# Kernel optimization log

Hardware: AMD Instinct MI355X
Metric: run time of the kernel (lower is better)

Reference implementation:

```python
import jax, jax.numpy as jnp
import numpy as np

D_ATOM, D_MODEL, H = 128, 512, 4
D_H = D_ATOM // H
D_FF = 4 * D_ATOM
EPS = 1e-5


def _ln(x, g, b):
    m = jnp.mean(x, axis=-1, keepdims=True)
    v = jnp.mean((x - m) ** 2, axis=-1, keepdims=True)
    return (x - m) / jnp.sqrt(v + EPS) * g + b


def setup_inputs() -> dict:
    key = jax.random.key(0)
    ks = jax.random.split(key, 20)
    B, N_ATOM, N_PAIRS, N_TOK = 2, 2048, 16384, 512
    c_atom = jax.random.normal(ks[0], (B, N_ATOM, D_ATOM), dtype=jnp.float32)
    p_lm = jax.random.normal(ks[1], (B, N_PAIRS, 16), dtype=jnp.float32)
    p_lm_idx = jax.random.randint(ks[2], (B, N_PAIRS, 2), 0, N_ATOM, dtype=jnp.int32)
    token_idx = jnp.sort(jax.random.randint(ks[3], (B, N_ATOM), 0, N_TOK, dtype=jnp.int32), axis=-1)
    s = 0.05
    w = lambda k, sh: jax.random.normal(k, sh, dtype=jnp.float32) * s
    return {
        'c_atom': c_atom, 'p_lm': p_lm, 'p_lm_idx': p_lm_idx,
        'token_idx': token_idx, 'n_tokens': N_TOK,
        'ln_attn_g': jnp.ones((D_ATOM,), jnp.float32), 'ln_attn_b': jnp.zeros((D_ATOM,), jnp.float32),
        'w_q': w(ks[4], (D_ATOM, D_ATOM)), 'w_k': w(ks[5], (D_ATOM, D_ATOM)),
        'w_v': w(ks[6], (D_ATOM, D_ATOM)), 'w_g': w(ks[7], (D_ATOM, D_ATOM)),
        'w_o': w(ks[8], (D_ATOM, D_ATOM)),
        'pb_w': w(ks[9], (16, H)), 'pb_b': jnp.zeros((H,), jnp.float32),
        'ln_ff_g': jnp.ones((D_ATOM,), jnp.float32), 'ln_ff_b': jnp.zeros((D_ATOM,), jnp.float32),
        'sw_w1': w(ks[10], (D_ATOM, D_FF)), 'sw_w2': w(ks[11], (D_ATOM, D_FF)),
        'sw_w3': w(ks[12], (D_FF, D_ATOM)),
        'tok_w': w(ks[13], (D_ATOM, D_MODEL)), 'tok_b': jnp.zeros((D_MODEL,), jnp.float32),
    }


def reference(c_atom, p_lm, p_lm_idx, token_idx, n_tokens,
              ln_attn_g, ln_attn_b, w_q, w_k, w_v, w_g, w_o, pb_w, pb_b,
              ln_ff_g, ln_ff_b, sw_w1, sw_w2, sw_w3, tok_w, tok_b):
    B, N, _ = c_atom.shape
    q_n = _ln(c_atom, ln_attn_g, ln_attn_b)
    Q = (q_n @ w_q).reshape(B, N, H, D_H)
    K = (q_n @ w_k).reshape(B, N, H, D_H)
    V = (q_n @ w_v).reshape(B, N, H, D_H)
    G = q_n @ w_g  # (B, N, d_atom)

    scores = jnp.einsum('bihd,bjhd->bhij', Q, K) / jnp.sqrt(jnp.float32(D_H))

    bias = p_lm @ pb_w + pb_b  # (B, P, H)
    def scat(src, dst, b_):
        return jnp.zeros((H, N, N), b_.dtype).at[:, src, dst].set(b_.T)
    pair_bias = jax.vmap(scat)(p_lm_idx[..., 0], p_lm_idx[..., 1], bias)
    scores = scores + pair_bias

    token_mask = token_idx[:, :, None] == token_idx[:, None, :]  # (B,N,N)
    scores = jnp.where(token_mask[:, None], scores, -jnp.inf)
    attn = jax.nn.softmax(scores, axis=-1)
    attn = jnp.nan_to_num(attn)

    att_out = jnp.einsum('bhij,bjhd->bihd', attn, V).reshape(B, N, D_ATOM)
    q = c_atom + jax.nn.sigmoid(G) * (att_out @ w_o)
    h = _ln(q, ln_ff_g, ln_ff_b)
    q = q + (jax.nn.silu(h @ sw_w1) * (h @ sw_w2)) @ sw_w3
    atom_feat = q @ tok_w + tok_b  # (B, N, d_model)

    seg = (token_idx + jnp.arange(B, dtype=token_idx.dtype)[:, None] * n_tokens).reshape(-1)
    sums = jax.ops.segment_sum(atom_feat.reshape(B * N, D_MODEL), seg, num_segments=B * n_tokens)
    cnts = jax.ops.segment_sum(jnp.ones((B * N,), atom_feat.dtype), seg, num_segments=B * n_tokens)
    out = sums / jnp.maximum(cnts, 1.0)[:, None]
    return out.reshape(B, n_tokens, D_MODEL)
```

## Files before the change

### kernel.cpp

```cpp
#include <hip/hip_runtime.h>
#include <hip/hip_bf16.h>
#include <math.h>

#define B_     2
#define N_     2048
#define DA     128
#define H_     4
#define DH     32
#define DFF    512
#define DM     512
#define NT     512
#define NP     16384
#define MAXL   32
#define LDSP   136

typedef short bf16x8 __attribute__((ext_vector_type(8)));
typedef float f32x4  __attribute__((ext_vector_type(4)));

__device__ __forceinline__ short bf16r(float x) {
    union { float f; unsigned u; } v; v.f = x;
    unsigned r = v.u + 0x7FFFu + ((v.u >> 16) & 1u);
    return (short)(r >> 16);
}
__device__ __forceinline__ float bf2f(short h) {
    union { unsigned u; float f; } v;
    v.u = ((unsigned)(unsigned short)h) << 16;
    return v.f;
}

__global__ __launch_bounds__(1024) void setup_kernel(
        const float* __restrict__ wq, const float* __restrict__ wk,
        const float* __restrict__ wv, const float* __restrict__ wg,
        const float* __restrict__ wo, const float* __restrict__ w1,
        const float* __restrict__ w2, const float* __restrict__ w3,
        const float* __restrict__ tw, const int* __restrict__ tok,
        const int* __restrict__ pidx,
        const float* __restrict__ c_atom, const float* __restrict__ lng,
        const float* __restrict__ lnb,
        short* __restrict__ pqkvg, short* __restrict__ pwo,
        short* __restrict__ pw12, short* __restrict__ pw3,
        short* __restrict__ ptok, short* __restrict__ hln,
        int* __restrict__ cnt, int* __restrict__ tst,
        int* __restrict__ win) {
    __shared__ int c[1024];
    __shared__ int sb[1024];
    if (blockIdx.x < 42) {
        int gid = blockIdx.x * 1024 + threadIdx.x;
        int lane = gid & 63;
        int grp = gid >> 6;
        int quad = lane >> 4, nn = lane & 15;
        const float* src; short* dst; int stride;
        if (grp < 128) {
            int g = grp; int kt = g & 3, nt = g >> 2;
            int n = nt * 16 + nn;
            const float* w = (n < 128) ? wq : (n < 256) ? wk : (n < 384) ? wv : wg;
            src = w + (kt * 32 + quad * 8) * 128 + (n & 127);
            dst = pqkvg + (g * 64 + lane) * 8;
            stride = 128;
        } else if (grp < 160) {
            int g = grp - 128; int kt = g & 3, nt = g >> 2;
            src = wo + (kt * 32 + quad * 8) * 128 + nt * 16 + nn;
            dst = pwo + (g * 64 + lane) * 8;
            stride = 128;
        } else if (grp < 416) {
            int g = grp - 160; int kt = g & 3, nt = g >> 2;
            int n = nt * 16 + nn;
            src = ((n & 1) ? w2 : w1) + (kt * 32 + quad * 8) * 512 + (n >> 1);
            dst = pw12 + (g * 64 + lane) * 8;
            stride = 512;
        } else if (grp < 544) {
            int g = grp - 416; int kt = g & 15, nt = g >> 4;
            src = w3 + (kt * 32 + quad * 8) * 128 + nt * 16 + nn;
            dst = pw3 + (g * 64 + lane) * 8;
            stride = 128;
        } else {
            int g = grp - 544; int kt = g & 3, nt = g >> 2;
            src = tw + (kt * 32 + quad * 8) * 512 + nt * 16 + nn;
            dst = ptok + (g * 64 + lane) * 8;
            stride = 512;
        }
#pragma unroll
        for (int j = 0; j < 8; j++) dst[j] = bf16r(src[j * stride]);
    } else if (blockIdx.x == 42) {
        int tid = threadIdx.x;
        c[tid] = 0;
        __syncthreads();
#pragma unroll
        for (int i = 0; i < 4; i++) {
            int idx = tid + i * 1024;
            int b = idx >> 11;
            atomicAdd(&c[b * NT + tok[idx]], 1);
        }
        __syncthreads();
        int t = tid & (NT - 1);
        int v = c[tid];
        int* cur = c;
        int* alt = sb;
        for (int d = 1; d < NT; d <<= 1) {
            int y = cur[tid];
            if (t >= d) y += cur[tid - d];
            alt[tid] = y;
            __syncthreads();
            int* tmp = cur; cur = alt; alt = tmp;
        }
        tst[tid] = cur[tid] - v;
        cnt[tid] = v;
    } else if (blockIdx.x < 75) {
        int p = (blockIdx.x - 43) * 1024 + threadIdx.x;
        int b = p >> 14, pp = p & (NP - 1);
        int src = pidx[p * 2], dst = pidx[p * 2 + 1];
        if (tok[b * N_ + src] == tok[b * N_ + dst])
            atomicMax(&win[(b * N_ + src) * MAXL + (dst & 31)], pp + 1);
    } else {
        int t = threadIdx.x;
        int rowg = (blockIdx.x - 75) * 256 + (t >> 2);
        int sub = t & 3;
        const float* xr = c_atom + rowg * DA + sub * 32;
        float4 v[8];
        float s = 0.f, sq = 0.f;
#pragma unroll
        for (int i = 0; i < 8; i++) {
            v[i] = *(const float4*)(xr + i * 4);
            s  += v[i].x + v[i].y + v[i].z + v[i].w;
            sq += v[i].x * v[i].x + v[i].y * v[i].y + v[i].z * v[i].z + v[i].w * v[i].w;
        }
        s += __shfl_xor(s, 1); sq += __shfl_xor(sq, 1);
        s += __shfl_xor(s, 2); sq += __shfl_xor(sq, 2);
        float mean = s * (1.f / 128.f);
        float var = sq * (1.f / 128.f) - mean * mean;
        float inv = rsqrtf(var + 1e-5f);
        const float* gp = lng + sub * 32;
        const float* bp = lnb + sub * 32;
        short* dst = hln + rowg * DA + sub * 32;
#pragma unroll
        for (int i = 0; i < 8; i++) {
            dst[i * 4 + 0] = bf16r((v[i].x - mean) * inv * gp[i * 4 + 0] + bp[i * 4 + 0]);
            dst[i * 4 + 1] = bf16r((v[i].y - mean) * inv * gp[i * 4 + 1] + bp[i * 4 + 1]);
            dst[i * 4 + 2] = bf16r((v[i].z - mean) * inv * gp[i * 4 + 2] + bp[i * 4 + 2]);
            dst[i * 4 + 3] = bf16r((v[i].w - mean) * inv * gp[i * 4 + 3] + bp[i * 4 + 3]);
        }
    }
}

template<int K, int NTT>
__device__ __forceinline__ void gemm_lds(const short* __restrict__ Alds,
                                         const short* __restrict__ Bp,
                                         int nt0, int lane, f32x4* acc) {
    constexpr int KT = K / 32;
    const short* arow = Alds + (lane & 15) * LDSP + (lane >> 4) * 8;
    const short* bbase = Bp + nt0 * KT * 512 + lane * 8;
#pragma unroll
    for (int kt = 0; kt < KT; kt++) {
        bf16x8 a = *(const bf16x8*)(arow + kt * 32);
#pragma unroll
        for (int nt = 0; nt < NTT; nt++) {
            bf16x8 b = *(const bf16x8*)(bbase + (nt * KT + kt) * 512);
            acc[nt] = __builtin_amdgcn_mfma_f32_16x16x32_bf16(a, b, acc[nt], 0, 0, 0);
        }
    }
}

template<int K, int NTT>
__device__ __forceinline__ void gemm_glb(const short* __restrict__ A,
                                         const short* __restrict__ Bp,
                                         int m0, int nt0, int lane, f32x4* acc) {
    constexpr int KT = K / 32;
    const short* arow = A + (m0 + (lane & 15)) * K + (lane >> 4) * 8;
    const short* bbase = Bp + nt0 * KT * 512 + lane * 8;
#pragma unroll
    for (int kt = 0; kt < KT; kt++) {
        bf16x8 a = *(const bf16x8*)(arow + kt * 32);
#pragma unroll
        for (int nt = 0; nt < NTT; nt++) {
            bf16x8 b = *(const bf16x8*)(bbase + (nt * KT + kt) * 512);
            acc[nt] = __builtin_amdgcn_mfma_f32_16x16x32_bf16(a, b, acc[nt], 0, 0, 0);
        }
    }
}

__global__ __launch_bounds__(256) void qkvg_mfma(const short* __restrict__ hln,
                                                 const short* __restrict__ Bp,
                                                 float* __restrict__ out) {
    int lane = threadIdx.x & 63;
    int wave = threadIdx.x >> 6;
    int m0 = blockIdx.x * 64 + wave * 16;
    int nt0 = blockIdx.y * 8;
    f32x4 acc[8];
#pragma unroll
    for (int i = 0; i < 8; i++)
#pragma unroll
        for (int r = 0; r < 4; r++) acc[i][r] = 0.f;
    gemm_glb<128, 8>(hln, Bp, m0, nt0, lane, acc);
    int r0 = m0 + ((lane >> 4) << 2);
    int cc = lane & 15;
#pragma unroll
    for (int nt = 0; nt < 8; nt++) {
        int col = (nt0 + nt) * 16 + cc;
#pragma unroll
        for (int r = 0; r < 4; r++) out[(r0 + r) * 512 + col] = acc[nt][r];
    }
}

__global__ __launch_bounds__(128) void attn_kernel(const float* __restrict__ qkvg,
                                                   const int* __restrict__ tok,
                                                   const int* __restrict__ tst,
                                                   const int* __restrict__ cnt,
                                                   const int* __restrict__ winner,
                                                   const float* __restrict__ plm,
                                                   const float* __restrict__ pbw,
                                                   const float* __restrict__ pbb,
                                                   short* __restrict__ atth) {
    __shared__ float sc[H_][MAXL];
    int blk = blockIdx.x;
    int b = blk >> 11;
    int h = threadIdx.x >> 5, d = threadIdx.x & 31;
    int t = tok[blk];
    int start = tst[b * NT + t];
    int L = cnt[b * NT + t];
    if (L > MAXL) L = MAXL;
    float qv = qkvg[blk * 512 + h * DH + d];
    const float* kbase = qkvg + (size_t)(b * N_ + start) * 512 + 128 + h * DH + d;
    const float* vbase = kbase + 128;
    const int* wbase = winner + blk * MAXL;
    const float scale = 0.17677669529663687f;
    for (int j0 = 0; j0 < L; j0 += 8) {
        int m = L - j0; if (m > 8) m = 8;
        float kv[8]; int pw[8];
#pragma unroll
        for (int u = 0; u < 8; u++) {
            if (u < m) {
                kv[u] = kbase[(j0 + u) * 512];
                pw[u] = wbase[(start + j0 + u) & 31];
            }
        }
#pragma unroll
        for (int u = 0; u < 8; u++) {
            if (u < m) {
                float s = qv * kv[u];
#pragma unroll
                for (int mm = 16; mm; mm >>= 1) s += __shfl_xor(s, mm, 32);
                s *= scale;
                if (pw[u] > 0) {
                    const float* pl = plm + (size_t)(b * NP + pw[u] - 1) * 16;
                    float bsum = pbb[h];
#pragma unroll
                    for (int f = 0; f < 16; f++) bsum += pl[f] * pbw[f * H_ + h];
                    s += bsum;
                }
                if (d == 0) sc[h][j0 + u] = s;
            }
        }
    }
    __syncthreads();
    float mx = -1e30f;
    for (int jj = 0; jj < L; jj++) mx = fmaxf(mx, sc[h][jj]);
    float denom = 0.f, acc = 0.f;
    for (int j0 = 0; j0 < L; j0 += 8) {
        int m = L - j0; if (m > 8) m = 8;
        float vv[8];
#pragma unroll
        for (int u = 0; u < 8; u++)
            if (u < m) vv[u] = vbase[(j0 + u) * 512];
#pragma unroll
        for (int u = 0; u < 8; u++) {
            if (u < m) {
                float pj = expf(sc[h][j0 + u] - mx);
                denom += pj;
                acc += pj * vv[u];
            }
        }
    }
    atth[blk * DA + h * DH + d] = bf16r(acc / denom);
}

__global__ __launch_bounds__(256) void oplnffn1_mfma(const short* __restrict__ atth,
                                                     const short* __restrict__ pwo,
                                                     const float* __restrict__ qkvg,
                                                     const float* __restrict__ c_atom,
                                                     const float* __restrict__ lg,
                                                     const float* __restrict__ lb,
                                                     const short* __restrict__ pw12,
                                                     float* __restrict__ qbuf,
                                                     short* __restrict__ u) {
    __shared__ short alds[64 * LDSP];
    int lane = threadIdx.x & 63;
    int wave = threadIdx.x >> 6;
    int base = blockIdx.x * 64;
    int m0 = base + wave * 16;
    int quad = lane >> 4, cc = lane & 15;

    f32x4 acc[8];
#pragma unroll
    for (int i = 0; i < 8; i++)
#pragma unroll
        for (int r = 0; r < 4; r++) acc[i][r] = 0.f;
    gemm_glb<128, 8>(atth, pwo, m0, 0, lane, acc);

    float rsum[4], rsq[4];
#pragma unroll
    for (int r = 0; r < 4; r++) {
        int row = m0 + quad * 4 + r;
        float s = 0.f, sq = 0.f;
#pragma unroll
        for (int nt = 0; nt < 8; nt++) {
            int col = nt * 16 + cc;
            float g = qkvg[row * 512 + 384 + col];
            float sg = 1.f / (1.f + expf(-g));
            float val = c_atom[row * DA + col] + sg * acc[nt][r];
            acc[nt][r] = val;
            s += val; sq += val * val;
            if (blockIdx.y == 0) qbuf[row * DA + col] = val;
        }
        rsum[r] = s; rsq[r] = sq;
    }
#pragma unroll
    for (int m = 1; m < 16; m <<= 1) {
#pragma unroll
        for (int r = 0; r < 4; r++) {
            rsum[r] += __shfl_xor(rsum[r], m);
            rsq[r]  += __shfl_xor(rsq[r], m);
        }
    }
#pragma unroll
    for (int r = 0; r < 4; r++) {
        float mean = rsum[r] * (1.f / 128.f);
        float var = rsq[r] * (1.f / 128.f) - mean * mean;
        float inv = rsqrtf(var + 1e-5f);
        int lrow = wave * 16 + quad * 4 + r;
#pragma unroll
        for (int nt = 0; nt < 8; nt++) {
            int col = nt * 16 + cc;
            alds[lrow * LDSP + col] = bf16r((acc[nt][r] - mean) * inv * lg[col] + lb[col]);
        }
    }
    __syncthreads();

    int nt0 = blockIdx.y * 16;
    f32x4 acc2[16];
#pragma unroll
    for (int i = 0; i < 16; i++)
#pragma unroll
        for (int r = 0; r < 4; r++) acc2[i][r] = 0.f;
    gemm_lds<128, 16>(alds + wave * 16 * LDSP, pw12, nt0, lane, acc2);
    int r0 = m0 + quad * 4;
#pragma unroll
    for (int nt = 0; nt < 16; nt++) {
        int col8 = (nt0 + nt) * 8 + (cc >> 1);
#pragma unroll
        for (int r = 0; r < 4; r++) {
            float v = acc2[nt][r];
            float p = __shfl_xor(v, 1);
            if (!(lane & 1)) {
                float sil = v / (1.f + expf(-v));
                u[(r0 + r) * DFF + col8] = bf16r(sil * p);
            }
        }
    }
}

__global__ __launch_bounds__(128) void ffn2_mfma(const short* __restrict__ u,
                                                 const short* __restrict__ Bp,
                                                 const float* __restrict__ qbuf,
                                                 short* __restrict__ q2h) {
    int lane = threadIdx.x & 63;
    int m0 = blockIdx.x * 32 + (threadIdx.x >> 6) * 16;
    int nt0 = blockIdx.y * 2;
    f32x4 acc[2];
#pragma unroll
    for (int i = 0; i < 2; i++)
#pragma unroll
        for (int r = 0; r < 4; r++) acc[i][r] = 0.f;
    gemm_glb<512, 2>(u, Bp, m0, nt0, lane, acc);
    int r0 = m0 + ((lane >> 4) << 2);
    int cc = lane & 15;
#pragma unroll
    for (int nt = 0; nt < 2; nt++) {
        int col = (nt0 + nt) * 16 + cc;
#pragma unroll
        for (int r = 0; r < 4; r++) {
            int row = r0 + r;
            q2h[row * DA + col] = bf16r(qbuf[row * DA + col] + acc[nt][r]);
        }
    }
}

__global__ __launch_bounds__(256) void tokmean_mfma(const short* __restrict__ q2h,
                                                    const int* __restrict__ tst,
                                                    const int* __restrict__ cnt,
                                                    const short* __restrict__ Bp,
                                                    const float* __restrict__ tb,
                                                    float* __restrict__ out) {
    __shared__ short alds[64 * LDSP];
    int tid = threadIdx.x;
    int tt = tid >> 2, sub = tid & 3;
    int token = blockIdx.x * 64 + tt;
    int start = tst[token], n = cnt[token];
    int b = token >> 9;
    float accm[32];
#pragma unroll
    for (int i = 0; i < 32; i++) accm[i] = 0.f;
    const short* rp = q2h + (size_t)(b * N_ + start) * DA + sub * 32;
    if (n > 0) {
        bf16x8 v[4];
#pragma unroll
        for (int v8 = 0; v8 < 4; v8++) v[v8] = *(const bf16x8*)(rp + v8 * 8);
        for (int a = 1; a <= n; a++) {
            bf16x8 nx[4];
            if (a < n) {
#pragma unroll
                for (int v8 = 0; v8 < 4; v8++) nx[v8] = *(const bf16x8*)(rp + a * DA + v8 * 8);
            }
#pragma unroll
            for (int v8 = 0; v8 < 4; v8++)
#pragma unroll
                for (int j = 0; j < 8; j++) accm[v8 * 8 + j] += bf2f(v[v8][j]);
            if (a < n) {
#pragma unroll
                for (int v8 = 0; v8 < 4; v8++) v[v8] = nx[v8];
            }
        }
    }
    float inv = (n > 0) ? 1.f / (float)n : 0.f;
    short* dst = alds + tt * LDSP + sub * 32;
#pragma unroll
    for (int i = 0; i < 32; i++) dst[i] = bf16r(accm[i] * inv);
    __syncthreads();

    int lane = tid & 63;
    int wave = tid >> 6;
    int nt0 = blockIdx.y * 4;
    f32x4 acc[4];
#pragma unroll
    for (int i = 0; i < 4; i++)
#pragma unroll
        for (int r = 0; r < 4; r++) acc[i][r] = 0.f;
    gemm_lds<128, 4>(alds + wave * 16 * LDSP, Bp, nt0, lane, acc);
    int r0 = blockIdx.x * 64 + wave * 16 + ((lane >> 4) << 2);
    int cc = lane & 15;
#pragma unroll
    for (int nt = 0; nt < 4; nt++) {
        int col = (nt0 + nt) * 16 + cc;
        float bv = tb[col];
#pragma unroll
        for (int r = 0; r < 4; r++) out[(size_t)(r0 + r) * DM + col] = acc[nt][r] + bv;
    }
}

extern "C" void kernel_launch(void* const* d_in, const int* in_sizes, int n_in,
                              void* d_out, int out_size, void* d_ws, size_t ws_size,
                              hipStream_t stream) {
    const float* c_atom  = (const float*)d_in[0];
    const float* p_lm    = (const float*)d_in[1];
    const int*   p_idx   = (const int*)d_in[2];
    const int*   tok     = (const int*)d_in[3];
    const float* ln_a_g  = (const float*)d_in[5];
    const float* ln_a_b  = (const float*)d_in[6];
    const float* w_q     = (const float*)d_in[7];
    const float* w_k     = (const float*)d_in[8];
    const float* w_v     = (const float*)d_in[9];
    const float* w_g     = (const float*)d_in[10];
    const float* w_o     = (const float*)d_in[11];
    const float* pb_w    = (const float*)d_in[12];
    const float* pb_b    = (const float*)d_in[13];
    const float* ln_f_g  = (const float*)d_in[14];
    const float* ln_f_b  = (const float*)d_in[15];
    const float* sw_w1   = (const float*)d_in[16];
    const float* sw_w2   = (const float*)d_in[17];
    const float* sw_w3   = (const float*)d_in[18];
    const float* tok_w   = (const float*)d_in[19];
    const float* tok_b   = (const float*)d_in[20];
    float* out = (float*)d_out;

    float* ws = (float*)d_ws;
    int*   cnt   = (int*)ws;
    int*   tst   = cnt + 1024;
    int*   win   = tst + 1024;
    short* pqkvg = (short*)(win + 131072);
    short* pwo   = pqkvg + 65536;
    short* pw12  = pwo + 16384;
    short* pw3   = pw12 + 131072;
    short* ptok  = pw3 + 65536;
    short* atth  = ptok + 65536;
    float* qbuf  = (float*)(atth + 524288);
    float* qkvg  = qbuf + 524288;
    short* uh    = (short*)(qkvg + 2097152);
    short* hln   = uh + 2097152;
    short* q2h   = atth;

    setup_kernel<<<91, 1024, 0, stream>>>(w_q, w_k, w_v, w_g, w_o, sw_w1, sw_w2,
                                          sw_w3, tok_w, tok, p_idx,
                                          c_atom, ln_a_g, ln_a_b,
                                          pqkvg, pwo, pw12, pw3, ptok, hln,
                                          cnt, tst, win);

    qkvg_mfma<<<dim3(64, 4), 256, 0, stream>>>(hln, pqkvg, qkvg);

    attn_kernel<<<B_ * N_, 128, 0, stream>>>(qkvg, tok, tst, cnt, win,
                                             p_lm, pb_w, pb_b, atth);

    oplnffn1_mfma<<<dim3(64, 4), 256, 0, stream>>>(atth, pwo, qkvg, c_atom,
                                                   ln_f_g, ln_f_b, pw12, qbuf, uh);

    ffn2_mfma<<<dim3(128, 4), 128, 0, stream>>>(uh, pw3, qbuf, q2h);

    tokmean_mfma<<<dim3(16, 8), 256, 0, stream>>>(q2h, tst, cnt, ptok, tok_b, out);
}
```

Baseline: 167.6 us.

## Fuse all stages into one cooperative persistent kernel with grid syncs

Replaces the six separate kernel launches with a single cooperative kernel of 256 blocks that runs setup, QKVG GEMM, attention, FFN and token-mean stages separated by grid-wide barriers. Each stage's work is remapped onto the fixed grid, and attention switches to an online softmax that reads K and V in one pass. This aims to remove launch overhead and inter-kernel gaps, at the cost of grid.sync barriers and a fixed grid that may underutilize the device in some stages.

```diff
diff --git a/kernel.cpp b/kernel.cpp
--- a/kernel.cpp
+++ b/kernel.cpp
@@ -1,6 +1,9 @@
 #include <hip/hip_runtime.h>
+#include <hip/hip_cooperative_groups.h>
 #include <hip/hip_bf16.h>
 #include <math.h>
+
+namespace cg = cooperative_groups;
 
 #define B_     2
 #define N_     2048
@@ -28,120 +31,6 @@
     return v.f;
 }
 
-__global__ __launch_bounds__(1024) void setup_kernel(
-        const float* __restrict__ wq, const float* __restrict__ wk,
-        const float* __restrict__ wv, const float* __restrict__ wg,
-        const float* __restrict__ wo, const float* __restrict__ w1,
-        const float* __restrict__ w2, const float* __restrict__ w3,
-        const float* __restrict__ tw, const int* __restrict__ tok,
-        const int* __restrict__ pidx,
-        const float* __restrict__ c_atom, const float* __restrict__ lng,
-        const float* __restrict__ lnb,
-        short* __restrict__ pqkvg, short* __restrict__ pwo,
-        short* __restrict__ pw12, short* __restrict__ pw3,
-        short* __restrict__ ptok, short* __restrict__ hln,
-        int* __restrict__ cnt, int* __restrict__ tst,
-        int* __restrict__ win) {
-    __shared__ int c[1024];
-    __shared__ int sb[1024];
-    if (blockIdx.x < 42) {
-        int gid = blockIdx.x * 1024 + threadIdx.x;
-        int lane = gid & 63;
-        int grp = gid >> 6;
-        int quad = lane >> 4, nn = lane & 15;
-        const float* src; short* dst; int stride;
-        if (grp < 128) {
-            int g = grp; int kt = g & 3, nt = g >> 2;
-            int n = nt * 16 + nn;
-            const float* w = (n < 128) ? wq : (n < 256) ? wk : (n < 384) ? wv : wg;
-            src = w + (kt * 32 + quad * 8) * 128 + (n & 127);
-            dst = pqkvg + (g * 64 + lane) * 8;
-            stride = 128;
-        } else if (grp < 160) {
-            int g = grp - 128; int kt = g & 3, nt = g >> 2;
-            src = wo + (kt * 32 + quad * 8) * 128 + nt * 16 + nn;
-            dst = pwo + (g * 64 + lane) * 8;
-            stride = 128;
-        } else if (grp < 416) {
-            int g = grp - 160; int kt = g & 3, nt = g >> 2;
-            int n = nt * 16 + nn;
-            src = ((n & 1) ? w2 : w1) + (kt * 32 + quad * 8) * 512 + (n >> 1);
-            dst = pw12 + (g * 64 + lane) * 8;
-            stride = 512;
-        } else if (grp < 544) {
-            int g = grp - 416; int kt = g & 15, nt = g >> 4;
-            src = w3 + (kt * 32 + quad * 8) * 128 + nt * 16 + nn;
-            dst = pw3 + (g * 64 + lane) * 8;
-            stride = 128;
-        } else {
-            int g = grp - 544; int kt = g & 3, nt = g >> 2;
-            src = tw + (kt * 32 + quad * 8) * 512 + nt * 16 + nn;
-            dst = ptok + (g * 64 + lane) * 8;
-            stride = 512;
-        }
-#pragma unroll
-        for (int j = 0; j < 8; j++) dst[j] = bf16r(src[j * stride]);
-    } else if (blockIdx.x == 42) {
-        int tid = threadIdx.x;
-        c[tid] = 0;
-        __syncthreads();
-#pragma unroll
-        for (int i = 0; i < 4; i++) {
-            int idx = tid + i * 1024;
-            int b = idx >> 11;
-            atomicAdd(&c[b * NT + tok[idx]], 1);
-        }
-        __syncthreads();
-        int t = tid & (NT - 1);
-        int v = c[tid];
-        int* cur = c;
-        int* alt = sb;
-        for (int d = 1; d < NT; d <<= 1) {
-            int y = cur[tid];
-            if (t >= d) y += cur[tid - d];
-            alt[tid] = y;
-            __syncthreads();
-            int* tmp = cur; cur = alt; alt = tmp;
-        }
-        tst[tid] = cur[tid] - v;
-        cnt[tid] = v;
-    } else if (blockIdx.x < 75) {
-        int p = (blockIdx.x - 43) * 1024 + threadIdx.x;
-        int b = p >> 14, pp = p & (NP - 1);
-        int src = pidx[p * 2], dst = pidx[p * 2 + 1];
-        if (tok[b * N_ + src] == tok[b * N_ + dst])
-            atomicMax(&win[(b * N_ + src) * MAXL + (dst & 31)], pp + 1);
-    } else {
-        int t = threadIdx.x;
-        int rowg = (blockIdx.x - 75) * 256 + (t >> 2);
-        int sub = t & 3;
-        const float* xr = c_atom + rowg * DA + sub * 32;
-        float4 v[8];
-        float s = 0.f, sq = 0.f;
-#pragma unroll
-        for (int i = 0; i < 8; i++) {
-            v[i] = *(const float4*)(xr + i * 4);
-            s  += v[i].x + v[i].y + v[i].z + v[i].w;
-            sq += v[i].x * v[i].x + v[i].y * v[i].y + v[i].z * v[i].z + v[i].w * v[i].w;
-        }
-        s += __shfl_xor(s, 1); sq += __shfl_xor(sq, 1);
-        s += __shfl_xor(s, 2); sq += __shfl_xor(sq, 2);
-        float mean = s * (1.f / 128.f);
-        float var = sq * (1.f / 128.f) - mean * mean;
-        float inv = rsqrtf(var + 1e-5f);
-        const float* gp = lng + sub * 32;
-        const float* bp = lnb + sub * 32;
-        short* dst = hln + rowg * DA + sub * 32;
-#pragma unroll
-        for (int i = 0; i < 8; i++) {
-            dst[i * 4 + 0] = bf16r((v[i].x - mean) * inv * gp[i * 4 + 0] + bp[i * 4 + 0]);
-            dst[i * 4 + 1] = bf16r((v[i].y - mean) * inv * gp[i * 4 + 1] + bp[i * 4 + 1]);
-            dst[i * 4 + 2] = bf16r((v[i].z - mean) * inv * gp[i * 4 + 2] + bp[i * 4 + 2]);
-            dst[i * 4 + 3] = bf16r((v[i].w - mean) * inv * gp[i * 4 + 3] + bp[i * 4 + 3]);
-        }
-    }
-}
-
 template<int K, int NTT>
 __device__ __forceinline__ void gemm_lds(const short* __restrict__ Alds,
                                          const short* __restrict__ Bp,
@@ -178,271 +67,351 @@
     }
 }
 
-__global__ __launch_bounds__(256) void qkvg_mfma(const short* __restrict__ hln,
-                                                 const short* __restrict__ Bp,
-                                                 float* __restrict__ out) {
-    int lane = threadIdx.x & 63;
-    int wave = threadIdx.x >> 6;
-    int m0 = blockIdx.x * 64 + wave * 16;
-    int nt0 = blockIdx.y * 8;
-    f32x4 acc[8];
-#pragma unroll
-    for (int i = 0; i < 8; i++)
-#pragma unroll
-        for (int r = 0; r < 4; r++) acc[i][r] = 0.f;
-    gemm_glb<128, 8>(hln, Bp, m0, nt0, lane, acc);
-    int r0 = m0 + ((lane >> 4) << 2);
-    int cc = lane & 15;
-#pragma unroll
-    for (int nt = 0; nt < 8; nt++) {
-        int col = (nt0 + nt) * 16 + cc;
-#pragma unroll
-        for (int r = 0; r < 4; r++) out[(r0 + r) * 512 + col] = acc[nt][r];
-    }
-}
-
-__global__ __launch_bounds__(128) void attn_kernel(const float* __restrict__ qkvg,
-                                                   const int* __restrict__ tok,
-                                                   const int* __restrict__ tst,
-                                                   const int* __restrict__ cnt,
-                                                   const int* __restrict__ winner,
-                                                   const float* __restrict__ plm,
-                                                   const float* __restrict__ pbw,
-                                                   const float* __restrict__ pbb,
-                                                   short* __restrict__ atth) {
-    __shared__ float sc[H_][MAXL];
+__global__ __launch_bounds__(512, 2) void mega(
+        const float* __restrict__ c_atom, const float* __restrict__ plm,
+        const int* __restrict__ pidx, const int* __restrict__ tok,
+        const float* __restrict__ lnag, const float* __restrict__ lnab,
+        const float* __restrict__ wq, const float* __restrict__ wk,
+        const float* __restrict__ wv, const float* __restrict__ wg,
+        const float* __restrict__ wo,
+        const float* __restrict__ pbw, const float* __restrict__ pbb,
+        const float* __restrict__ lnfg, const float* __restrict__ lnfb,
+        const float* __restrict__ w1, const float* __restrict__ w2,
+        const float* __restrict__ w3, const float* __restrict__ tw,
+        const float* __restrict__ tb,
+        float* __restrict__ out,
+        int* __restrict__ cnt, int* __restrict__ tst, int* __restrict__ win,
+        short* __restrict__ pqkvg, short* __restrict__ pwo,
+        short* __restrict__ pw12, short* __restrict__ pw3,
+        short* __restrict__ ptok,
+        short* __restrict__ hln, short* __restrict__ atth,
+        float* __restrict__ qbuf, float* __restrict__ qkvg,
+        short* __restrict__ uh) {
+    __shared__ __align__(16) char smraw[128 * LDSP * 2];
+    cg::grid_group grid = cg::this_grid();
     int blk = blockIdx.x;
-    int b = blk >> 11;
-    int h = threadIdx.x >> 5, d = threadIdx.x & 31;
-    int t = tok[blk];
-    int start = tst[b * NT + t];
-    int L = cnt[b * NT + t];
-    if (L > MAXL) L = MAXL;
-    float qv = qkvg[blk * 512 + h * DH + d];
-    const float* kbase = qkvg + (size_t)(b * N_ + start) * 512 + 128 + h * DH + d;
-    const float* vbase = kbase + 128;
-    const int* wbase = winner + blk * MAXL;
-    const float scale = 0.17677669529663687f;
-    for (int j0 = 0; j0 < L; j0 += 8) {
-        int m = L - j0; if (m > 8) m = 8;
-        float kv[8]; int pw[8];
-#pragma unroll
-        for (int u = 0; u < 8; u++) {
-            if (u < m) {
-                kv[u] = kbase[(j0 + u) * 512];
-                pw[u] = wbase[(start + j0 + u) & 31];
-            }
-        }
-#pragma unroll
-        for (int u = 0; u < 8; u++) {
-            if (u < m) {
-                float s = qv * kv[u];
-#pragma unroll
-                for (int mm = 16; mm; mm >>= 1) s += __shfl_xor(s, mm, 32);
-                s *= scale;
-                if (pw[u] > 0) {
-                    const float* pl = plm + (size_t)(b * NP + pw[u] - 1) * 16;
-                    float bsum = pbb[h];
-#pragma unroll
-                    for (int f = 0; f < 16; f++) bsum += pl[f] * pbw[f * H_ + h];
-                    s += bsum;
+    int tid = threadIdx.x;
+    int lane = tid & 63, wave = tid >> 6;
+
+    if (blk < 84) {
+        int g = blk * 8 + wave;
+        int quad = lane >> 4, nn = lane & 15;
+        const float* src; short* dst; int stride;
+        if (g < 128) {
+            int kt = g & 3, nt = g >> 2;
+            int n = nt * 16 + nn;
+            const float* w = (n < 128) ? wq : (n < 256) ? wk : (n < 384) ? wv : wg;
+            src = w + (kt * 32 + quad * 8) * 128 + (n & 127);
+            dst = pqkvg + (g * 64 + lane) * 8;
+            stride = 128;
+        } else if (g < 160) {
+            int gg = g - 128; int kt = gg & 3, nt = gg >> 2;
+            src = wo + (kt * 32 + quad * 8) * 128 + nt * 16 + nn;
+            dst = pwo + (gg * 64 + lane) * 8;
+            stride = 128;
+        } else if (g < 416) {
+            int gg = g - 160; int kt = gg & 3, nt = gg >> 2;
+            int n = nt * 16 + nn;
+            src = ((n & 1) ? w2 : w1) + (kt * 32 + quad * 8) * 512 + (n >> 1);
+            dst = pw12 + (gg * 64 + lane) * 8;
+            stride = 512;
+        } else if (g < 544) {
+            int gg = g - 416; int kt = gg & 15, nt = gg >> 4;
+            src = w3 + (kt * 32 + quad * 8) * 128 + nt * 16 + nn;
+            dst = pw3 + (gg * 64 + lane) * 8;
+            stride = 128;
+        } else {
+            int gg = g - 544; int kt = gg & 3, nt = gg >> 2;
+            src = tw + (kt * 32 + quad * 8) * 512 + nt * 16 + nn;
+            dst = ptok + (gg * 64 + lane) * 8;
+            stride = 512;
+        }
+#pragma unroll
+        for (int j = 0; j < 8; j++) dst[j] = bf16r(src[j * stride]);
+    } else if (blk < 116) {
+        int rowg = (blk - 84) * 128 + (tid >> 2);
+        int sub = tid & 3;
+        const float* xr = c_atom + rowg * DA + sub * 32;
+        float4 v[8];
+        float s = 0.f, sq = 0.f;
+#pragma unroll
+        for (int i = 0; i < 8; i++) {
+            v[i] = *(const float4*)(xr + i * 4);
+            s  += v[i].x + v[i].y + v[i].z + v[i].w;
+            sq += v[i].x * v[i].x + v[i].y * v[i].y + v[i].z * v[i].z + v[i].w * v[i].w;
+        }
+        s += __shfl_xor(s, 1); sq += __shfl_xor(sq, 1);
+        s += __shfl_xor(s, 2); sq += __shfl_xor(sq, 2);
+        float mean = s * (1.f / 128.f);
+        float var = sq * (1.f / 128.f) - mean * mean;
+        float inv = rsqrtf(var + 1e-5f);
+        const float* gp = lnag + sub * 32;
+        const float* bp = lnab + sub * 32;
+        short* dst = hln + rowg * DA + sub * 32;
+#pragma unroll
+        for (int i = 0; i < 8; i++) {
+            dst[i * 4 + 0] = bf16r((v[i].x - mean) * inv * gp[i * 4 + 0] + bp[i * 4 + 0]);
+            dst[i * 4 + 1] = bf16r((v[i].y - mean) * inv * gp[i * 4 + 1] + bp[i * 4 + 1]);
+            dst[i * 4 + 2] = bf16r((v[i].z - mean) * inv * gp[i * 4 + 2] + bp[i * 4 + 2]);
+            dst[i * 4 + 3] = bf16r((v[i].w - mean) * inv * gp[i * 4 + 3] + bp[i * 4 + 3]);
+        }
+    } else if (blk == 116) {
+        int* c  = (int*)smraw;
+        int* sb = c + 1024;
+        c[tid] = 0; c[tid + 512] = 0;
+        __syncthreads();
+#pragma unroll
+        for (int i = 0; i < 8; i++) {
+            int idx = tid + i * 512;
+            int b = idx >> 11;
+            atomicAdd(&c[b * NT + tok[idx]], 1);
+        }
+        __syncthreads();
+        int v0 = c[tid], v1 = c[tid + 512];
+        int* cur = c;
+        int* alt = sb;
+        for (int d = 1; d < 512; d <<= 1) {
+            int y0 = cur[tid];       if (tid >= d) y0 += cur[tid - d];
+            int y1 = cur[tid + 512]; if (tid >= d) y1 += cur[tid + 512 - d];
+            alt[tid] = y0; alt[tid + 512] = y1;
+            __syncthreads();
+            int* t_ = cur; cur = alt; alt = t_;
+        }
+        tst[tid] = cur[tid] - v0;          cnt[tid] = v0;
+        tst[tid + 512] = cur[tid + 512] - v1; cnt[tid + 512] = v1;
+    } else if (blk < 133) {
+        int base = (blk - 117) * 2048;
+#pragma unroll
+        for (int i = 0; i < 4; i++) {
+            int p = base + i * 512 + tid;
+            int b = p >> 14, pp = p & (NP - 1);
+            int src = pidx[p * 2], dst = pidx[p * 2 + 1];
+            if (tok[b * N_ + src] == tok[b * N_ + dst])
+                atomicMax(&win[(b * N_ + src) * MAXL + (dst & 31)], pp + 1);
+        }
+    }
+    grid.sync();
+
+    {
+        int xb = blk & 63, yb = blk >> 6;
+        int m0 = xb * 64 + (wave & 3) * 16;
+        int nt0 = yb * 8 + (wave >> 2) * 4;
+        f32x4 acc[4];
+#pragma unroll
+        for (int i = 0; i < 4; i++)
+#pragma unroll
+            for (int r = 0; r < 4; r++) acc[i][r] = 0.f;
+        gemm_glb<128, 4>(hln, pqkvg, m0, nt0, lane, acc);
+        int r0 = m0 + ((lane >> 4) << 2);
+        int cc = lane & 15;
+#pragma unroll
+        for (int nt = 0; nt < 4; nt++) {
+            int col = (nt0 + nt) * 16 + cc;
+#pragma unroll
+            for (int r = 0; r < 4; r++) qkvg[(r0 + r) * 512 + col] = acc[nt][r];
+        }
+    }
+    grid.sync();
+
+    {
+        int team = tid >> 7;
+        int t127 = tid & 127;
+        int h = t127 >> 5, d = t127 & 31;
+        const float scale = 0.17677669529663687f;
+        for (int i = 0; i < 4; i++) {
+            int atom = blk * 16 + team * 4 + i;
+            int b = atom >> 11;
+            int t = tok[atom];
+            int start = tst[b * NT + t];
+            int L = cnt[b * NT + t];
+            if (L > MAXL) L = MAXL;
+            float qv = qkvg[atom * 512 + h * DH + d];
+            const float* kbase = qkvg + (size_t)(b * N_ + start) * 512 + 128 + h * DH + d;
+            const float* vbase = kbase + 128;
+            const int* wbase = win + atom * MAXL;
+            float mrun = -1e30f, denom = 0.f, acc = 0.f;
+            for (int j0 = 0; j0 < L; j0 += 8) {
+                int m8 = L - j0; if (m8 > 8) m8 = 8;
+                float kv[8], vv[8]; int pw[8];
+#pragma unroll
+                for (int u = 0; u < 8; u++) {
+                    if (u < m8) {
+                        kv[u] = kbase[(j0 + u) * 512];
+                        vv[u] = vbase[(j0 + u) * 512];
+                        pw[u] = wbase[(start + j0 + u) & 31];
+                    }
                 }
-                if (d == 0) sc[h][j0 + u] = s;
-            }
-        }
-    }
-    __syncthreads();
-    float mx = -1e30f;
-    for (int jj = 0; jj < L; jj++) mx = fmaxf(mx, sc[h][jj]);
-    float denom = 0.f, acc = 0.f;
-    for (int j0 = 0; j0 < L; j0 += 8) {
-        int m = L - j0; if (m > 8) m = 8;
-        float vv[8];
-#pragma unroll
-        for (int u = 0; u < 8; u++)
-            if (u < m) vv[u] = vbase[(j0 + u) * 512];
-#pragma unroll
-        for (int u = 0; u < 8; u++) {
-            if (u < m) {
-                float pj = expf(sc[h][j0 + u] - mx);
-                denom += pj;
-                acc += pj * vv[u];
-            }
-        }
-    }
-    atth[blk * DA + h * DH + d] = bf16r(acc / denom);
-}
-
-__global__ __launch_bounds__(256) void oplnffn1_mfma(const short* __restrict__ atth,
-                                                     const short* __restrict__ pwo,
-                                                     const float* __restrict__ qkvg,
-                                                     const float* __restrict__ c_atom,
-                                                     const float* __restrict__ lg,
-                                                     const float* __restrict__ lb,
-                                                     const short* __restrict__ pw12,
-                                                     float* __restrict__ qbuf,
-                                                     short* __restrict__ u) {
-    __shared__ short alds[64 * LDSP];
-    int lane = threadIdx.x & 63;
-    int wave = threadIdx.x >> 6;
-    int base = blockIdx.x * 64;
-    int m0 = base + wave * 16;
-    int quad = lane >> 4, cc = lane & 15;
-
-    f32x4 acc[8];
-#pragma unroll
-    for (int i = 0; i < 8; i++)
-#pragma unroll
-        for (int r = 0; r < 4; r++) acc[i][r] = 0.f;
-    gemm_glb<128, 8>(atth, pwo, m0, 0, lane, acc);
-
-    float rsum[4], rsq[4];
-#pragma unroll
-    for (int r = 0; r < 4; r++) {
-        int row = m0 + quad * 4 + r;
-        float s = 0.f, sq = 0.f;
+                float s[8];
+#pragma unroll
+                for (int u = 0; u < 8; u++) {
+                    if (u < m8) {
+                        float sv = qv * kv[u];
+#pragma unroll
+                        for (int mm = 16; mm; mm >>= 1) sv += __shfl_xor(sv, mm, 32);
+                        sv *= scale;
+                        if (pw[u] > 0) {
+                            const float* pl = plm + (size_t)(b * NP + pw[u] - 1) * 16;
+                            float bsum = pbb[h];
+#pragma unroll
+                            for (int f = 0; f < 16; f++) bsum += pl[f] * pbw[f * H_ + h];
+                            sv += bsum;
+                        }
+                        s[u] = sv;
+                    }
+                }
+                float cmax = -1e30f;
+#pragma unroll
+                for (int u = 0; u < 8; u++)
+                    if (u < m8) cmax = fmaxf(cmax, s[u]);
+                float mnew = fmaxf(mrun, cmax);
+                float rs = expf(mrun - mnew);
+                denom *= rs; acc *= rs;
+#pragma unroll
+                for (int u = 0; u < 8; u++) {
+                    if (u < m8) {
+                        float p = expf(s[u] - mnew);
+                        denom += p;
+                        acc += p * vv[u];
+                    }
+                }
+                mrun = mnew;
+            }
+            atth[atom * DA + h * DH + d] = bf16r(acc / denom);
+        }
+    }
+    grid.sync();
+
+    {
+        short* alds = (short*)smraw;
+        int xb = blk & 31, yb = blk >> 5;
+        int m0 = xb * 128 + wave * 16;
+        int quad = lane >> 4, cc = lane & 15;
+        f32x4 acc[8];
+#pragma unroll
+        for (int i = 0; i < 8; i++)
+#pragma unroll
+            for (int r = 0; r < 4; r++) acc[i][r] = 0.f;
+        gemm_glb<128, 8>(atth, pwo, m0, 0, lane, acc);
+        float rsum[4], rsq[4];
+#pragma unroll
+        for (int r = 0; r < 4; r++) {
+            int row = m0 + quad * 4 + r;
+            float s = 0.f, sq = 0.f;
+#pragma unroll
+            for (int nt = 0; nt < 8; nt++) {
+                int col = nt * 16 + cc;
+                float g = qkvg[row * 512 + 384 + col];
+                float sg = 1.f / (1.f + expf(-g));
+                float val = c_atom[row * DA + col] + sg * acc[nt][r];
+                acc[nt][r] = val;
+                s += val; sq += val * val;
+                if (yb == 0) qbuf[row * DA + col] = val;
+            }
+            rsum[r] = s; rsq[r] = sq;
+        }
+#pragma unroll
+        for (int m = 1; m < 16; m <<= 1) {
+#pragma unroll
+            for (int r = 0; r < 4; r++) {
+                rsum[r] += __shfl_xor(rsum[r], m);
+                rsq[r]  += __shfl_xor(rsq[r], m);
+            }
+        }
+#pragma unroll
+        for (int r = 0; r < 4; r++) {
+            float mean = rsum[r] * (1.f / 128.f);
+            float var = rsq[r] * (1.f / 128.f) - mean * mean;
+            float inv = rsqrtf(var + 1e-5f);
+            int lrow = wave * 16 + quad * 4 + r;
+#pragma unroll
+            for (int nt = 0; nt < 8; nt++) {
+                int col = nt * 16 + cc;
+                alds[lrow * LDSP + col] = bf16r((acc[nt][r] - mean) * inv * lnfg[col] + lnfb[col]);
+            }
+        }
+        __syncthreads();
+        int nt0 = yb * 8;
+        f32x4 acc2[8];
+#pragma unroll
+        for (int i = 0; i < 8; i++)
+#pragma unroll
+            for (int r = 0; r < 4; r++) acc2[i][r] = 0.f;
+        gemm_lds<128, 8>(alds + wave * 16 * LDSP, pw12, nt0, lane, acc2);
+        int r0 = m0 + quad * 4;
 #pragma unroll
         for (int nt = 0; nt < 8; nt++) {
-            int col = nt * 16 + cc;
-            float g = qkvg[row * 512 + 384 + col];
-            float sg = 1.f / (1.f + expf(-g));
-            float val = c_atom[row * DA + col] + sg * acc[nt][r];
-            acc[nt][r] = val;
-            s += val; sq += val * val;
-            if (blockIdx.y == 0) qbuf[row * DA + col] = val;
-        }
-        rsum[r] = s; rsq[r] = sq;
-    }
-#pragma unroll
-    for (int m = 1; m < 16; m <<= 1) {
-#pragma unroll
-        for (int r = 0; r < 4; r++) {
-            rsum[r] += __shfl_xor(rsum[r], m);
-            rsq[r]  += __shfl_xor(rsq[r], m);
-        }
-    }
-#pragma unroll
-    for (int r = 0; r < 4; r++) {
-        float mean = rsum[r] * (1.f / 128.f);
-        float var = rsq[r] * (1.f / 128.f) - mean * mean;
-        float inv = rsqrtf(var + 1e-5f);
-        int lrow = wave * 16 + quad * 4 + r;
-#pragma unroll
-        for (int nt = 0; nt < 8; nt++) {
-            int col = nt * 16 + cc;
-            alds[lrow * LDSP + col] = bf16r((acc[nt][r] - mean) * inv * lg[col] + lb[col]);
-        }
-    }
-    __syncthreads();
-
-    int nt0 = blockIdx.y * 16;
-    f32x4 acc2[16];
-#pragma unroll
-    for (int i = 0; i < 16; i++)
-#pragma unroll
-        for (int r = 0; r < 4; r++) acc2[i][r] = 0.f;
-    gemm_lds<128, 16>(alds + wave * 16 * LDSP, pw12, nt0, lane, acc2);
-    int r0 = m0 + quad * 4;
-#pragma unroll
-    for (int nt = 0; nt < 16; nt++) {
-        int col8 = (nt0 + nt) * 8 + (cc >> 1);
-#pragma unroll
-        for (int r = 0; r < 4; r++) {
-            float v = acc2[nt][r];
-            float p = __shfl_xor(v, 1);
-            if (!(lane & 1)) {
-                float sil = v / (1.f + expf(-v));
-                u[(r0 + r) * DFF + col8] = bf16r(sil * p);
-            }
-        }
-    }
-}
-
-__global__ __launch_bounds__(128) void ffn2_mfma(const short* __restrict__ u,
-                                                 const short* __restrict__ Bp,
-                                                 const float* __restrict__ qbuf,
-                                                 short* __restrict__ q2h) {
-    int lane = threadIdx.x & 63;
-    int m0 = blockIdx.x * 32 + (threadIdx.x >> 6) * 16;
-    int nt0 = blockIdx.y * 2;
-    f32x4 acc[2];
-#pragma unroll
-    for (int i = 0; i < 2; i++)
-#pragma unroll
-        for (int r = 0; r < 4; r++) acc[i][r] = 0.f;
-    gemm_glb<512, 2>(u, Bp, m0, nt0, lane, acc);
-    int r0 = m0 + ((lane >> 4) << 2);
-    int cc = lane & 15;
-#pragma unroll
-    for (int nt = 0; nt < 2; nt++) {
-        int col = (nt0 + nt) * 16 + cc;
+            int col8 = (nt0 + nt) * 8 + (cc >> 1);
+#pragma unroll
+            for (int r = 0; r < 4; r++) {
+                float v = acc2[nt][r];
+                float p = __shfl_xor(v, 1);
+                if (!(lane & 1)) {
+                    float sil = v / (1.f + expf(-v));
+                    uh[(r0 + r) * DFF + col8] = bf16r(sil * p);
+                }
+            }
+        }
+    }
+    grid.sync();
+
+    {
+        short* q2h = atth;
+        int m0 = blk * 16;
+        int nt0 = wave;
+        f32x4 acc[1];
+#pragma unroll
+        for (int r = 0; r < 4; r++) acc[0][r] = 0.f;
+        gemm_glb<512, 1>(uh, pw3, m0, nt0, lane, acc);
+        int r0 = m0 + ((lane >> 4) << 2);
+        int cc = lane & 15;
+        int col = nt0 * 16 + cc;
 #pragma unroll
         for (int r = 0; r < 4; r++) {
             int row = r0 + r;
-            q2h[row * DA + col] = bf16r(qbuf[row * DA + col] + acc[nt][r]);
-        }
-    }
-}
-
-__global__ __launch_bounds__(256) void tokmean_mfma(const short* __restrict__ q2h,
-                                                    const int* __restrict__ tst,
-                                                    const int* __restrict__ cnt,
-                                                    const short* __restrict__ Bp,
-                                                    const float* __restrict__ tb,
-                                                    float* __restrict__ out) {
-    __shared__ short alds[64 * LDSP];
-    int tid = threadIdx.x;
-    int tt = tid >> 2, sub = tid & 3;
-    int token = blockIdx.x * 64 + tt;
-    int start = tst[token], n = cnt[token];
-    int b = token >> 9;
-    float accm[32];
-#pragma unroll
-    for (int i = 0; i < 32; i++) accm[i] = 0.f;
-    const short* rp = q2h + (size_t)(b * N_ + start) * DA + sub * 32;
-    if (n > 0) {
-        bf16x8 v[4];
-#pragma unroll
-        for (int v8 = 0; v8 < 4; v8++) v[v8] = *(const bf16x8*)(rp + v8 * 8);
-        for (int a = 1; a <= n; a++) {
-            bf16x8 nx[4];
-            if (a < n) {
-#pragma unroll
-                for (int v8 = 0; v8 < 4; v8++) nx[v8] = *(const bf16x8*)(rp + a * DA + v8 * 8);
-            }
-#pragma unroll
-            for (int v8 = 0; v8 < 4; v8++)
-#pragma unroll
-                for (int j = 0; j < 8; j++) accm[v8 * 8 + j] += bf2f(v[v8][j]);
-            if (a < n) {
-#pragma unroll
-                for (int v8 = 0; v8 < 4; v8++) v[v8] = nx[v8];
-            }
-        }
-    }
-    float inv = (n > 0) ? 1.f / (float)n : 0.f;
-    short* dst = alds + tt * LDSP + sub * 32;
-#pragma unroll
-    for (int i = 0; i < 32; i++) dst[i] = bf16r(accm[i] * inv);
-    __syncthreads();
-
-    int lane = tid & 63;
-    int wave = tid >> 6;
-    int nt0 = blockIdx.y * 4;
-    f32x4 acc[4];
-#pragma unroll
-    for (int i = 0; i < 4; i++)
-#pragma unroll
-        for (int r = 0; r < 4; r++) acc[i][r] = 0.f;
-    gemm_lds<128, 4>(alds + wave * 16 * LDSP, Bp, nt0, lane, acc);
-    int r0 = blockIdx.x * 64 + wave * 16 + ((lane >> 4) << 2);
-    int cc = lane & 15;
-#pragma unroll
-    for (int nt = 0; nt < 4; nt++) {
-        int col = (nt0 + nt) * 16 + cc;
+            q2h[row * DA + col] = bf16r(qbuf[row * DA + col] + acc[0][r]);
+        }
+    }
+    grid.sync();
+
+    {
+        const short* q2h = atth;
+        short* alds = (short*)smraw;
+        int xb = blk & 15, yb = blk >> 4;
+        int tt = tid >> 3, sub = tid & 7;
+        int token = xb * 64 + tt;
+        int start = tst[token], n = cnt[token];
+        int b = token >> 9;
+        float accm[16];
+#pragma unroll
+        for (int i = 0; i < 16; i++) accm[i] = 0.f;
+        const short* rp = q2h + (size_t)(b * N_ + start) * DA + sub * 16;
+        for (int a = 0; a < n; a++) {
+            bf16x8 v0 = *(const bf16x8*)(rp + a * DA);
+            bf16x8 v1 = *(const bf16x8*)(rp + a * DA + 8);
+#pragma unroll
+            for (int j = 0; j < 8; j++) {
+                accm[j]     += bf2f(v0[j]);
+                accm[8 + j] += bf2f(v1[j]);
+            }
+        }
+        float inv = (n > 0) ? 1.f / (float)n : 0.f;
+        short* dst = alds + tt * LDSP + sub * 16;
+#pragma unroll
+        for (int i = 0; i < 16; i++) dst[i] = bf16r(accm[i] * inv);
+        __syncthreads();
+
+        int nt0 = yb * 2 + (wave >> 2);
+        f32x4 acc[1];
+#pragma unroll
+        for (int r = 0; r < 4; r++) acc[0][r] = 0.f;
+        gemm_lds<128, 1>(alds + (wave & 3) * 16 * LDSP, ptok, nt0, lane, acc);
+        int r0 = xb * 64 + (wave & 3) * 16 + ((lane >> 4) << 2);
+        int cc = lane & 15;
+        int col = nt0 * 16 + cc;
         float bv = tb[col];
 #pragma unroll
-        for (int r = 0; r < 4; r++) out[(size_t)(r0 + r) * DM + col] = acc[nt][r] + bv;
+        for (int r = 0; r < 4; r++)
+            out[(size_t)(r0 + r) * DM + col] = acc[0][r] + bv;
     }
 }
 
@@ -485,23 +454,18 @@
     float* qkvg  = qbuf + 524288;
     short* uh    = (short*)(qkvg + 2097152);
     short* hln   = uh + 2097152;
-    short* q2h   = atth;
-
-    setup_kernel<<<91, 1024, 0, stream>>>(w_q, w_k, w_v, w_g, w_o, sw_w1, sw_w2,
-                                          sw_w3, tok_w, tok, p_idx,
-                                          c_atom, ln_a_g, ln_a_b,
-                                          pqkvg, pwo, pw12, pw3, ptok, hln,
-                                          cnt, tst, win);
-
-    qkvg_mfma<<<dim3(64, 4), 256, 0, stream>>>(hln, pqkvg, qkvg);
-
-    attn_kernel<<<B_ * N_, 128, 0, stream>>>(qkvg, tok, tst, cnt, win,
-                                             p_lm, pb_w, pb_b, atth);
-
-    oplnffn1_mfma<<<dim3(64, 4), 256, 0, stream>>>(atth, pwo, qkvg, c_atom,
-                                                   ln_f_g, ln_f_b, pw12, qbuf, uh);
-
-    ffn2_mfma<<<dim3(128, 4), 128, 0, stream>>>(uh, pw3, qbuf, q2h);
-
-    tokmean_mfma<<<dim3(16, 8), 256, 0, stream>>>(q2h, tst, cnt, ptok, tok_b, out);
-}
+
+    void* kargs[] = {
+        (void*)&c_atom, (void*)&p_lm, (void*)&p_idx, (void*)&tok,
+        (void*)&ln_a_g, (void*)&ln_a_b,
+        (void*)&w_q, (void*)&w_k, (void*)&w_v, (void*)&w_g, (void*)&w_o,
+        (void*)&pb_w, (void*)&pb_b, (void*)&ln_f_g, (void*)&ln_f_b,
+        (void*)&sw_w1, (void*)&sw_w2, (void*)&sw_w3, (void*)&tok_w, (void*)&tok_b,
+        (void*)&out,
+        (void*)&cnt, (void*)&tst, (void*)&win,
+        (void*)&pqkvg, (void*)&pwo, (void*)&pw12, (void*)&pw3, (void*)&ptok,
+        (void*)&hln, (void*)&atth, (void*)&qbuf, (void*)&qkvg, (void*)&uh };
+
+    hipLaunchCooperativeKernel((const void*)mega, dim3(256), dim3(512),
+                               kargs, 0, stream);
+}
```

Measured after the change: 334.5 us. +99.6%, slower.
